# Performance work log

Hardware: AMD Instinct MI355X
Metric: run time of the kernel (lower is better)

Reference implementation:

```python
import jax, jax.numpy as jnp
import numpy as np

HEADS = 16
SEQ_LEN = 2048
EMB = 1024
BATCH = 2


def setup_inputs() -> dict:
    key = jax.random.key(0)
    ks = jax.random.split(key, 5)
    s = 1.0 / np.sqrt(EMB)
    return {
        "x": jax.random.normal(ks[0], (BATCH, SEQ_LEN, EMB), dtype=jnp.float32),
        "Wk": jax.random.normal(ks[1], (EMB, EMB), dtype=jnp.float32) * s,
        "Wq": jax.random.normal(ks[2], (EMB, EMB), dtype=jnp.float32) * s,
        "Wv": jax.random.normal(ks[3], (EMB, EMB), dtype=jnp.float32) * s,
        "Wu": jax.random.normal(ks[4], (EMB, EMB), dtype=jnp.float32) * s,
        "bu": jnp.zeros((EMB,), dtype=jnp.float32),
    }


def reference(x, Wk, Wq, Wv, Wu, bu):
    B, S, E = x.shape
    H = HEADS
    D = E // H
    # projections (torch Linear: y = x @ W.T); split heads -> [B, H, S, D]
    def proj(W):
        return (x @ W.T).reshape(B, S, H, D).transpose(0, 2, 1, 3)
    q, k, v = proj(Wq), proj(Wk), proj(Wv)
    scores = jnp.einsum("bhsd,bhtd->bhst", q, k) / jnp.sqrt(jnp.float32(D))
    causal_mask = jnp.triu(jnp.ones((S, S), dtype=bool), k=1)  # True above diag
    scores = jnp.where(causal_mask, -jnp.inf, scores)
    attn = jax.nn.softmax(scores, axis=-1)
    ctx = jnp.einsum("bhst,bhtd->bhsd", attn, v)  # [B,H,S,D]
    out = ctx.transpose(0, 2, 1, 3).reshape(B, S, E)
    return out @ Wu.T + bu
```

## Files before the change

### kernel.cpp

```cpp
#include <hip/hip_runtime.h>
#include <hip/hip_bf16.h>

#define HEADS 16
#define SEQ   2048
#define EMB   1024
#define BATCH 2
#define DHEAD 64
#define MTOK  (BATCH * SEQ)

typedef __bf16 bf16x8 __attribute__((ext_vector_type(8)));
typedef float  floatx4 __attribute__((ext_vector_type(4)));

__device__ __forceinline__ void gl_lds16(const void* g, void* l) {
  __builtin_amdgcn_global_load_lds((__attribute__((address_space(1))) void*)(g),
                                   (__attribute__((address_space(3))) void*)(l), 16, 0, 0);
}

__device__ __forceinline__ unsigned short f2bf(float f) {
  __bf16 h = (__bf16)f;
  return __builtin_bit_cast(unsigned short, h);
}

__global__ __launch_bounds__(256) void cvt_kernel(
    const float* __restrict__ x,  const float* __restrict__ wq,
    const float* __restrict__ wk, const float* __restrict__ wv,
    const float* __restrict__ wu,
    unsigned short* __restrict__ xb,  unsigned short* __restrict__ wqb,
    unsigned short* __restrict__ wkb, unsigned short* __restrict__ wvb,
    unsigned short* __restrict__ wub) {
  const int g = blockIdx.x * 256 + threadIdx.x;
  const int XG = (MTOK * EMB) / 4;
  const int WG = (EMB * EMB) / 4;
  const float* src; unsigned short* dst; int off;
  if (g < XG) { src = x; dst = xb; off = g; }
  else {
    int t = g - XG; int wsel = t / WG; off = t - wsel * WG;
    const float* ss[4] = {wq, wk, wv, wu};
    unsigned short* dd[4] = {wqb, wkb, wvb, wub};
    src = ss[wsel]; dst = dd[wsel];
  }
  float4 v = ((const float4*)src)[off];
  ushort4 o;
  o.x = f2bf(v.x); o.y = f2bf(v.y); o.z = f2bf(v.z); o.w = f2bf(v.w);
  ((ushort4*)dst)[off] = o;
}

__global__ __launch_bounds__(256) void gemm_qkv(
    const unsigned short* __restrict__ xb,
    const unsigned short* __restrict__ wqb, const unsigned short* __restrict__ wkb,
    const unsigned short* __restrict__ wvb,
    unsigned short* __restrict__ Qb, unsigned short* __restrict__ Kb,
    unsigned short* __restrict__ Vt) {
  constexpr int BM = 128, BN = 128, BK = 64;
  __shared__ unsigned short As[BM * BK];
  __shared__ unsigned short Bs[BN * BK];
  const int z = blockIdx.z;
  const unsigned short* W = (z == 0) ? wqb : (z == 1) ? wkb : wvb;
  const int m0 = blockIdx.x * BM, n0 = blockIdx.y * BN;
  const int tid = threadIdx.x, w = tid >> 6, lane = tid & 63;
  const int quad = lane >> 4, l16 = lane & 15;
  const int wm = w >> 1, wn = w & 1;
  const int srow = lane >> 3;
  const int scol = ((lane & 7) ^ srow) * 8;

  floatx4 acc[4][4] = {};

  for (int kt = 0; kt < EMB / BK; ++kt) {
    const int k0 = kt * BK;
#pragma unroll
    for (int i = 0; i < 4; ++i) {
      int r0 = i * 32 + w * 8;
      gl_lds16(xb + (size_t)(m0 + r0 + srow) * EMB + k0 + scol, &As[r0 * BK]);
      gl_lds16(W  + (size_t)(n0 + r0 + srow) * EMB + k0 + scol, &Bs[r0 * BK]);
    }
    __syncthreads();
    bf16x8 af[4][2], bfv[4][2];
#pragma unroll
    for (int mb = 0; mb < 4; ++mb) {
      int ra = wm * 64 + mb * 16 + l16;
#pragma unroll
      for (int ks = 0; ks < 2; ++ks)
        af[mb][ks] = *(const bf16x8*)&As[ra * BK + (((ks * 4 + quad) ^ (ra & 7)) * 8)];
    }
#pragma unroll
    for (int nb = 0; nb < 4; ++nb) {
      int rb = wn * 64 + nb * 16 + l16;
#pragma unroll
      for (int ks = 0; ks < 2; ++ks)
        bfv[nb][ks] = *(const bf16x8*)&Bs[rb * BK + (((ks * 4 + quad) ^ (rb & 7)) * 8)];
    }
#pragma unroll
    for (int ks = 0; ks < 2; ++ks)
#pragma unroll
      for (int mb = 0; mb < 4; ++mb)
#pragma unroll
        for (int nb = 0; nb < 4; ++nb)
          acc[mb][nb] = __builtin_amdgcn_mfma_f32_16x16x32_bf16(af[mb][ks], bfv[nb][ks], acc[mb][nb], 0, 0, 0);
    __syncthreads();
  }

  if (z < 2) {
    unsigned short* C = (z == 0) ? Qb : Kb;
    const float scale = (z == 0) ? 0.180336876f : 1.0f;
#pragma unroll
    for (int mb = 0; mb < 4; ++mb) {
#pragma unroll
      for (int nb = 0; nb < 4; ++nb) {
        int n = n0 + wn * 64 + nb * 16 + l16;
#pragma unroll
        for (int r = 0; r < 4; ++r) {
          int m = m0 + wm * 64 + mb * 16 + quad * 4 + r;
          C[(size_t)m * EMB + n] = f2bf(acc[mb][nb][r] * scale);
        }
      }
    }
  } else {
#pragma unroll
    for (int mb = 0; mb < 4; ++mb) {
      int mbase = m0 + wm * 64 + mb * 16 + quad * 4;
      int b = mbase >> 11, s = mbase & (SEQ - 1);
#pragma unroll
      for (int nb = 0; nb < 4; ++nb) {
        int n = n0 + wn * 64 + nb * 16 + l16;
        ushort4 o;
        o.x = f2bf(acc[mb][nb][0]); o.y = f2bf(acc[mb][nb][1]);
        o.z = f2bf(acc[mb][nb][2]); o.w = f2bf(acc[mb][nb][3]);
        *(ushort4*)&Vt[((size_t)b * (HEADS * DHEAD) + n) * SEQ + s] = o;
      }
    }
  }
}

__global__ __launch_bounds__(256) void attn_kernel(
    const unsigned short* __restrict__ Qb, const unsigned short* __restrict__ Kb,
    const unsigned short* __restrict__ Vt, unsigned short* __restrict__ ctx) {
  constexpr int KT = 128;
  constexpr int PST = KT + 8;
  __shared__ unsigned short Ks[KT * DHEAD];
  __shared__ unsigned short Vs[DHEAD * KT];
  __shared__ __bf16 Ps[4 * 16 * PST];
  const int pair = blockIdx.x, bh = blockIdx.y;
  const int b = bh >> 4, h = bh & 15;
  const int tid = threadIdx.x, w = tid >> 6, lane = tid & 63;
  const int quad = lane >> 4, l16 = lane & 15;

  const unsigned short* Kbh = Kb + (size_t)b * SEQ * EMB + h * DHEAD;
  const unsigned short* Vbh = Vt + (size_t)bh * DHEAD * SEQ;
  __bf16* Pw = &Ps[w * (16 * PST)];

  int kq[4], kd[4], vd[4], vk[4];
#pragma unroll
  for (int i = 0; i < 4; ++i) {
    int c = i * 256 + tid;
    kq[i] = ((c >> 6) & 7) * 16 + (c & 15);
    kd[i] = ((c >> 9) << 5) + (((c >> 4) & 3) << 3);
    vd[i] = (((c >> 6) & 3) << 4) + (c & 15);
    vk[i] = (((c >> 8) & 3) << 5) + (((c >> 4) & 3) << 3);
  }

  for (int pi = 0; pi < 2; ++pi) {
    const int qt = pi ? (31 - pair) : pair;
    const int q0 = qt * 64;
    const int myrow = q0 + w * 16 + quad * 4;

    const size_t qrow = (size_t)(b * SEQ + q0 + w * 16 + l16) * EMB + h * DHEAD;
    bf16x8 qf[2];
    qf[0] = *(const bf16x8*)&Qb[qrow + quad * 8];
    qf[1] = *(const bf16x8*)&Qb[qrow + 32 + quad * 8];

    float lsum[4] = {0.0f, 0.0f, 0.0f, 0.0f};
    floatx4 acc_o[4] = {};

    const int nkt = (qt + 2) >> 1;
    for (int ktile = 0; ktile < nkt; ++ktile) {
      const int kt0 = ktile * KT;
#pragma unroll
      for (int i = 0; i < 4; ++i) {
        gl_lds16(Kbh + (size_t)(kt0 + kq[i]) * EMB + kd[i], &Ks[(i * 256 + w * 64) * 8]);
        gl_lds16(Vbh + (size_t)vd[i] * SEQ + kt0 + vk[i], &Vs[(i * 256 + w * 64) * 8]);
      }
      __syncthreads();

      floatx4 accs[8] = {};
#pragma unroll
      for (int ks = 0; ks < 2; ++ks)
#pragma unroll
        for (int nb = 0; nb < 8; ++nb) {
          bf16x8 kf = *(const bf16x8*)&Ks[((ks * 8 + nb) * 64 + lane) * 8];
          accs[nb] = __builtin_amdgcn_mfma_f32_16x16x32_bf16(qf[ks], kf, accs[nb], 0, 0, 0);
        }

      if (ktile == nkt - 1) {
#pragma unroll
        for (int nb = 0; nb < 8; ++nb) {
          int col = kt0 + nb * 16 + l16;
#pragma unroll
          for (int r = 0; r < 4; ++r)
            if (col > myrow + r) accs[nb][r] = -1e30f;
        }
      }

#pragma unroll
      for (int r = 0; r < 4; ++r) {
#pragma unroll
        for (int nb = 0; nb < 8; ++nb) {
          float pe = exp2f(accs[nb][r]);
          Pw[(quad * 4 + r) * PST + nb * 16 + l16] = (__bf16)pe;
          lsum[r] += pe;
        }
      }

#pragma unroll
      for (int ks = 0; ks < 4; ++ks) {
        bf16x8 pf = *(const bf16x8*)&Pw[l16 * PST + ks * 32 + quad * 8];
#pragma unroll
        for (int nb = 0; nb < 4; ++nb) {
          bf16x8 vf = *(const bf16x8*)&Vs[((ks * 4 + nb) * 64 + lane) * 8];
          acc_o[nb] = __builtin_amdgcn_mfma_f32_16x16x32_bf16(pf, vf, acc_o[nb], 0, 0, 0);
        }
      }
      __syncthreads();
    }

#pragma unroll
    for (int r = 0; r < 4; ++r) {
      float rs = lsum[r];
      rs += __shfl_xor(rs, 1);
      rs += __shfl_xor(rs, 2);
      rs += __shfl_xor(rs, 4);
      rs += __shfl_xor(rs, 8);
      float inv = 1.0f / rs;
      size_t base = (size_t)(b * SEQ + myrow + r) * EMB + h * DHEAD;
#pragma unroll
      for (int nb = 0; nb < 4; ++nb)
        ctx[base + nb * 16 + l16] = f2bf(acc_o[nb][r] * inv);
    }
  }
}

__global__ __launch_bounds__(256) void gemm_out(
    const unsigned short* __restrict__ ctx, const unsigned short* __restrict__ wub,
    const float* __restrict__ bu, float* __restrict__ out) {
  constexpr int BM = 128, BN = 64, BK = 64;
  __shared__ unsigned short As[BM * BK];
  __shared__ unsigned short Bs[BN * BK];
  const int m0 = blockIdx.x * BM, n0 = blockIdx.y * BN;
  const int tid = threadIdx.x, w = tid >> 6, lane = tid & 63;
  const int quad = lane >> 4, l16 = lane & 15;
  const int wm = w >> 1, wn = w & 1;
  const int srow = lane >> 3;
  const int scol = ((lane & 7) ^ srow) * 8;

  floatx4 acc[4][2] = {};

  for (int kt = 0; kt < EMB / BK; ++kt) {
    const int k0 = kt * BK;
#pragma unroll
    for (int i = 0; i < 4; ++i) {
      int r0 = i * 32 + w * 8;
      gl_lds16(ctx + (size_t)(m0 + r0 + srow) * EMB + k0 + scol, &As[r0 * BK]);
    }
#pragma unroll
    for (int i = 0; i < 2; ++i) {
      int r0 = i * 32 + w * 8;
      gl_lds16(wub + (size_t)(n0 + r0 + srow) * EMB + k0 + scol, &Bs[r0 * BK]);
    }
    __syncthreads();
    bf16x8 af[4][2], bfv[2][2];
#pragma unroll
    for (int mb = 0; mb < 4; ++mb) {
      int ra = wm * 64 + mb * 16 + l16;
#pragma unroll
      for (int ks = 0; ks < 2; ++ks)
        af[mb][ks] = *(const bf16x8*)&As[ra * BK + (((ks * 4 + quad) ^ (ra & 7)) * 8)];
    }
#pragma unroll
    for (int nb = 0; nb < 2; ++nb) {
      int rb = wn * 32 + nb * 16 + l16;
#pragma unroll
      for (int ks = 0; ks < 2; ++ks)
        bfv[nb][ks] = *(const bf16x8*)&Bs[rb * BK + (((ks * 4 + quad) ^ (rb & 7)) * 8)];
    }
#pragma unroll
    for (int ks = 0; ks < 2; ++ks)
#pragma unroll
      for (int mb = 0; mb < 4; ++mb)
#pragma unroll
        for (int nb = 0; nb < 2; ++nb)
          acc[mb][nb] = __builtin_amdgcn_mfma_f32_16x16x32_bf16(af[mb][ks], bfv[nb][ks], acc[mb][nb], 0, 0, 0);
    __syncthreads();
  }

#pragma unroll
  for (int mb = 0; mb < 4; ++mb) {
#pragma unroll
    for (int nb = 0; nb < 2; ++nb) {
      int n = n0 + wn * 32 + nb * 16 + l16;
      float bias = bu[n];
#pragma unroll
      for (int r = 0; r < 4; ++r) {
        int m = m0 + wm * 64 + mb * 16 + quad * 4 + r;
        out[(size_t)m * EMB + n] = acc[mb][nb][r] + bias;
      }
    }
  }
}

extern "C" void kernel_launch(void* const* d_in, const int* in_sizes, int n_in,
                              void* d_out, int out_size, void* d_ws, size_t ws_size,
                              hipStream_t stream) {
  const float* x  = (const float*)d_in[0];
  const float* Wk = (const float*)d_in[1];
  const float* Wq = (const float*)d_in[2];
  const float* Wv = (const float*)d_in[3];
  const float* Wu = (const float*)d_in[4];
  const float* bu = (const float*)d_in[5];

  char* ws = (char*)d_ws;
  const size_t MB1 = 1 << 20;
  unsigned short* xb  = (unsigned short*)(ws + 0);
  unsigned short* wqb = (unsigned short*)(ws + 8  * MB1);
  unsigned short* wkb = (unsigned short*)(ws + 10 * MB1);
  unsigned short* wvb = (unsigned short*)(ws + 12 * MB1);
  unsigned short* wub = (unsigned short*)(ws + 14 * MB1);
  unsigned short* Qb  = (unsigned short*)(ws + 16 * MB1);
  unsigned short* Kb  = (unsigned short*)(ws + 24 * MB1);
  unsigned short* Vt  = (unsigned short*)(ws + 32 * MB1);
  unsigned short* ctx = (unsigned short*)(ws + 40 * MB1);

  cvt_kernel<<<8192, 256, 0, stream>>>(x, Wq, Wk, Wv, Wu, xb, wqb, wkb, wvb, wub);
  gemm_qkv<<<dim3(32, 8, 3), 256, 0, stream>>>(xb, wqb, wkb, wvb, Qb, Kb, Vt);
  attn_kernel<<<dim3(16, 32), 256, 0, stream>>>(Qb, Kb, Vt, ctx);
  gemm_out<<<dim3(32, 16), 256, 0, stream>>>(ctx, wub, bu, (float*)d_out);
}
```

Measured before the change: 189.7 us.

## Fuse QKV weight tiles per block and split attention into per-tile blocks

The QKV GEMM now loads one shared x tile and three 64-wide weight tiles (Q, K, V) per block, so x is staged once for all three projections instead of three times. The grid changes from 32x8x3 to 32x16. The attention kernel drops the paired-tile scheme and launches one block per 64-row query tile, in reverse order so the longest tiles start first, with 64-wide K/V tiles and simpler load indexing. This raises attention block count and parallelism, but each block does more iterations with smaller tiles and more barriers.

Result: slower. 219.8 us (+15.9%).

```diff
diff --git a/kernel.cpp b/kernel.cpp
--- a/kernel.cpp
+++ b/kernel.cpp
@@ -51,19 +51,18 @@
     const unsigned short* __restrict__ wvb,
     unsigned short* __restrict__ Qb, unsigned short* __restrict__ Kb,
     unsigned short* __restrict__ Vt) {
-  constexpr int BM = 128, BN = 128, BK = 64;
+  constexpr int BM = 128, BN = 64, BK = 64;
   __shared__ unsigned short As[BM * BK];
-  __shared__ unsigned short Bs[BN * BK];
-  const int z = blockIdx.z;
-  const unsigned short* W = (z == 0) ? wqb : (z == 1) ? wkb : wvb;
+  __shared__ unsigned short Bs[3 * BN * BK];
   const int m0 = blockIdx.x * BM, n0 = blockIdx.y * BN;
   const int tid = threadIdx.x, w = tid >> 6, lane = tid & 63;
   const int quad = lane >> 4, l16 = lane & 15;
   const int wm = w >> 1, wn = w & 1;
   const int srow = lane >> 3;
   const int scol = ((lane & 7) ^ srow) * 8;
-
-  floatx4 acc[4][4] = {};
+  const unsigned short* Ws[3] = {wqb, wkb, wvb};
+
+  floatx4 acc[3][4][2] = {};
 
   for (int kt = 0; kt < EMB / BK; ++kt) {
     const int k0 = kt * BK;
@@ -71,62 +70,70 @@
     for (int i = 0; i < 4; ++i) {
       int r0 = i * 32 + w * 8;
       gl_lds16(xb + (size_t)(m0 + r0 + srow) * EMB + k0 + scol, &As[r0 * BK]);
-      gl_lds16(W  + (size_t)(n0 + r0 + srow) * EMB + k0 + scol, &Bs[r0 * BK]);
-    }
-    __syncthreads();
-    bf16x8 af[4][2], bfv[4][2];
-#pragma unroll
-    for (int mb = 0; mb < 4; ++mb) {
-      int ra = wm * 64 + mb * 16 + l16;
-#pragma unroll
-      for (int ks = 0; ks < 2; ++ks)
-        af[mb][ks] = *(const bf16x8*)&As[ra * BK + (((ks * 4 + quad) ^ (ra & 7)) * 8)];
-    }
-#pragma unroll
-    for (int nb = 0; nb < 4; ++nb) {
-      int rb = wn * 64 + nb * 16 + l16;
-#pragma unroll
-      for (int ks = 0; ks < 2; ++ks)
-        bfv[nb][ks] = *(const bf16x8*)&Bs[rb * BK + (((ks * 4 + quad) ^ (rb & 7)) * 8)];
-    }
-#pragma unroll
-    for (int ks = 0; ks < 2; ++ks)
-#pragma unroll
-      for (int mb = 0; mb < 4; ++mb)
-#pragma unroll
-        for (int nb = 0; nb < 4; ++nb)
-          acc[mb][nb] = __builtin_amdgcn_mfma_f32_16x16x32_bf16(af[mb][ks], bfv[nb][ks], acc[mb][nb], 0, 0, 0);
-    __syncthreads();
-  }
-
-  if (z < 2) {
+    }
+#pragma unroll
+    for (int z = 0; z < 3; ++z)
+#pragma unroll
+      for (int i = 0; i < 2; ++i) {
+        int r0 = i * 32 + w * 8;
+        gl_lds16(Ws[z] + (size_t)(n0 + r0 + srow) * EMB + k0 + scol,
+                 &Bs[z * (BN * BK) + r0 * BK]);
+      }
+    __syncthreads();
+#pragma unroll
+    for (int ks = 0; ks < 2; ++ks) {
+      bf16x8 af[4];
+#pragma unroll
+      for (int mb = 0; mb < 4; ++mb) {
+        int ra = wm * 64 + mb * 16 + l16;
+        af[mb] = *(const bf16x8*)&As[ra * BK + (((ks * 4 + quad) ^ (ra & 7)) * 8)];
+      }
+#pragma unroll
+      for (int z = 0; z < 3; ++z) {
+        bf16x8 bfv[2];
+#pragma unroll
+        for (int nb = 0; nb < 2; ++nb) {
+          int rb = wn * 32 + nb * 16 + l16;
+          bfv[nb] = *(const bf16x8*)&Bs[z * (BN * BK) + rb * BK + (((ks * 4 + quad) ^ (rb & 7)) * 8)];
+        }
+#pragma unroll
+        for (int mb = 0; mb < 4; ++mb)
+#pragma unroll
+          for (int nb = 0; nb < 2; ++nb)
+            acc[z][mb][nb] = __builtin_amdgcn_mfma_f32_16x16x32_bf16(af[mb], bfv[nb], acc[z][mb][nb], 0, 0, 0);
+      }
+    }
+    __syncthreads();
+  }
+
+#pragma unroll
+  for (int z = 0; z < 2; ++z) {
     unsigned short* C = (z == 0) ? Qb : Kb;
     const float scale = (z == 0) ? 0.180336876f : 1.0f;
 #pragma unroll
     for (int mb = 0; mb < 4; ++mb) {
 #pragma unroll
-      for (int nb = 0; nb < 4; ++nb) {
-        int n = n0 + wn * 64 + nb * 16 + l16;
+      for (int nb = 0; nb < 2; ++nb) {
+        int n = n0 + wn * 32 + nb * 16 + l16;
 #pragma unroll
         for (int r = 0; r < 4; ++r) {
           int m = m0 + wm * 64 + mb * 16 + quad * 4 + r;
-          C[(size_t)m * EMB + n] = f2bf(acc[mb][nb][r] * scale);
+          C[(size_t)m * EMB + n] = f2bf(acc[z][mb][nb][r] * scale);
         }
       }
     }
-  } else {
-#pragma unroll
-    for (int mb = 0; mb < 4; ++mb) {
-      int mbase = m0 + wm * 64 + mb * 16 + quad * 4;
-      int b = mbase >> 11, s = mbase & (SEQ - 1);
-#pragma unroll
-      for (int nb = 0; nb < 4; ++nb) {
-        int n = n0 + wn * 64 + nb * 16 + l16;
-        ushort4 o;
-        o.x = f2bf(acc[mb][nb][0]); o.y = f2bf(acc[mb][nb][1]);
-        o.z = f2bf(acc[mb][nb][2]); o.w = f2bf(acc[mb][nb][3]);
-        *(ushort4*)&Vt[((size_t)b * (HEADS * DHEAD) + n) * SEQ + s] = o;
-      }
+  }
+#pragma unroll
+  for (int mb = 0; mb < 4; ++mb) {
+    int mbase = m0 + wm * 64 + mb * 16 + quad * 4;
+    int b = mbase >> 11, s = mbase & (SEQ - 1);
+#pragma unroll
+    for (int nb = 0; nb < 2; ++nb) {
+      int n = n0 + wn * 32 + nb * 16 + l16;
+      ushort4 o;
+      o.x = f2bf(acc[2][mb][nb][0]); o.y = f2bf(acc[2][mb][nb][1]);
+      o.z = f2bf(acc[2][mb][nb][2]); o.w = f2bf(acc[2][mb][nb][3]);
+      *(ushort4*)&Vt[((size_t)b * (HEADS * DHEAD) + n) * SEQ + s] = o;
     }
   }
 }
@@ -134,13 +141,14 @@
 __global__ __launch_bounds__(256) void attn_kernel(
     const unsigned short* __restrict__ Qb, const unsigned short* __restrict__ Kb,
     const unsigned short* __restrict__ Vt, unsigned short* __restrict__ ctx) {
-  constexpr int KT = 128;
-  constexpr int PST = KT + 8;
+  constexpr int KT = 64;
+  constexpr int PST = KT + 12;
   __shared__ unsigned short Ks[KT * DHEAD];
   __shared__ unsigned short Vs[DHEAD * KT];
   __shared__ __bf16 Ps[4 * 16 * PST];
-  const int pair = blockIdx.x, bh = blockIdx.y;
+  const int qt = 31 - blockIdx.x, bh = blockIdx.y;
   const int b = bh >> 4, h = bh & 15;
+  const int q0 = qt * 64;
   const int tid = threadIdx.x, w = tid >> 6, lane = tid & 63;
   const int quad = lane >> 4, l16 = lane & 15;
 
@@ -148,93 +156,80 @@
   const unsigned short* Vbh = Vt + (size_t)bh * DHEAD * SEQ;
   __bf16* Pw = &Ps[w * (16 * PST)];
 
-  int kq[4], kd[4], vd[4], vk[4];
-#pragma unroll
-  for (int i = 0; i < 4; ++i) {
-    int c = i * 256 + tid;
-    kq[i] = ((c >> 6) & 7) * 16 + (c & 15);
-    kd[i] = ((c >> 9) << 5) + (((c >> 4) & 3) << 3);
-    vd[i] = (((c >> 6) & 3) << 4) + (c & 15);
-    vk[i] = (((c >> 8) & 3) << 5) + (((c >> 4) & 3) << 3);
-  }
-
-  for (int pi = 0; pi < 2; ++pi) {
-    const int qt = pi ? (31 - pair) : pair;
-    const int q0 = qt * 64;
-    const int myrow = q0 + w * 16 + quad * 4;
-
-    const size_t qrow = (size_t)(b * SEQ + q0 + w * 16 + l16) * EMB + h * DHEAD;
-    bf16x8 qf[2];
-    qf[0] = *(const bf16x8*)&Qb[qrow + quad * 8];
-    qf[1] = *(const bf16x8*)&Qb[qrow + 32 + quad * 8];
-
-    float lsum[4] = {0.0f, 0.0f, 0.0f, 0.0f};
-    floatx4 acc_o[4] = {};
-
-    const int nkt = (qt + 2) >> 1;
-    for (int ktile = 0; ktile < nkt; ++ktile) {
-      const int kt0 = ktile * KT;
-#pragma unroll
-      for (int i = 0; i < 4; ++i) {
-        gl_lds16(Kbh + (size_t)(kt0 + kq[i]) * EMB + kd[i], &Ks[(i * 256 + w * 64) * 8]);
-        gl_lds16(Vbh + (size_t)vd[i] * SEQ + kt0 + vk[i], &Vs[(i * 256 + w * 64) * 8]);
-      }
-      __syncthreads();
-
-      floatx4 accs[8] = {};
-#pragma unroll
-      for (int ks = 0; ks < 2; ++ks)
-#pragma unroll
-        for (int nb = 0; nb < 8; ++nb) {
-          bf16x8 kf = *(const bf16x8*)&Ks[((ks * 8 + nb) * 64 + lane) * 8];
-          accs[nb] = __builtin_amdgcn_mfma_f32_16x16x32_bf16(qf[ks], kf, accs[nb], 0, 0, 0);
-        }
-
-      if (ktile == nkt - 1) {
-#pragma unroll
-        for (int nb = 0; nb < 8; ++nb) {
-          int col = kt0 + nb * 16 + l16;
-#pragma unroll
-          for (int r = 0; r < 4; ++r)
-            if (col > myrow + r) accs[nb][r] = -1e30f;
-        }
-      }
-
-#pragma unroll
-      for (int r = 0; r < 4; ++r) {
-#pragma unroll
-        for (int nb = 0; nb < 8; ++nb) {
-          float pe = exp2f(accs[nb][r]);
-          Pw[(quad * 4 + r) * PST + nb * 16 + l16] = (__bf16)pe;
-          lsum[r] += pe;
-        }
-      }
-
-#pragma unroll
-      for (int ks = 0; ks < 4; ++ks) {
-        bf16x8 pf = *(const bf16x8*)&Pw[l16 * PST + ks * 32 + quad * 8];
-#pragma unroll
-        for (int nb = 0; nb < 4; ++nb) {
-          bf16x8 vf = *(const bf16x8*)&Vs[((ks * 4 + nb) * 64 + lane) * 8];
-          acc_o[nb] = __builtin_amdgcn_mfma_f32_16x16x32_bf16(pf, vf, acc_o[nb], 0, 0, 0);
-        }
-      }
-      __syncthreads();
+  const int krow = w * 16 + l16;
+  const int dc0 = quad * 8, dc1 = 32 + quad * 8;
+
+  const int myrow = q0 + w * 16 + quad * 4;
+  const size_t qrow = (size_t)(b * SEQ + q0 + w * 16 + l16) * EMB + h * DHEAD;
+  bf16x8 qf[2];
+  qf[0] = *(const bf16x8*)&Qb[qrow + quad * 8];
+  qf[1] = *(const bf16x8*)&Qb[qrow + 32 + quad * 8];
+
+  float lsum[4] = {0.0f, 0.0f, 0.0f, 0.0f};
+  floatx4 acc_o[4] = {};
+
+  const int nkt = qt + 1;
+  for (int ktile = 0; ktile < nkt; ++ktile) {
+    const int kt0 = ktile * KT;
+    gl_lds16(Kbh + (size_t)(kt0 + krow) * EMB + dc0, &Ks[(w * 64 + lane) * 8]);
+    gl_lds16(Kbh + (size_t)(kt0 + krow) * EMB + dc1, &Ks[((4 + w) * 64 + lane) * 8]);
+    gl_lds16(Vbh + (size_t)krow * SEQ + kt0 + dc0, &Vs[(w * 64 + lane) * 8]);
+    gl_lds16(Vbh + (size_t)krow * SEQ + kt0 + dc1, &Vs[((4 + w) * 64 + lane) * 8]);
+    __syncthreads();
+
+    floatx4 accs[4] = {};
+#pragma unroll
+    for (int ks = 0; ks < 2; ++ks)
+#pragma unroll
+      for (int nb = 0; nb < 4; ++nb) {
+        bf16x8 kf = *(const bf16x8*)&Ks[((ks * 4 + nb) * 64 + lane) * 8];
+        accs[nb] = __builtin_amdgcn_mfma_f32_16x16x32_bf16(qf[ks], kf, accs[nb], 0, 0, 0);
+      }
+
+    if (ktile == nkt - 1) {
+#pragma unroll
+      for (int nb = 0; nb < 4; ++nb) {
+        int col = kt0 + nb * 16 + l16;
+#pragma unroll
+        for (int r = 0; r < 4; ++r)
+          if (col > myrow + r) accs[nb][r] = -1e30f;
+      }
     }
 
 #pragma unroll
     for (int r = 0; r < 4; ++r) {
-      float rs = lsum[r];
-      rs += __shfl_xor(rs, 1);
-      rs += __shfl_xor(rs, 2);
-      rs += __shfl_xor(rs, 4);
-      rs += __shfl_xor(rs, 8);
-      float inv = 1.0f / rs;
-      size_t base = (size_t)(b * SEQ + myrow + r) * EMB + h * DHEAD;
-#pragma unroll
-      for (int nb = 0; nb < 4; ++nb)
-        ctx[base + nb * 16 + l16] = f2bf(acc_o[nb][r] * inv);
-    }
+#pragma unroll
+      for (int nb = 0; nb < 4; ++nb) {
+        float pe = exp2f(accs[nb][r]);
+        Pw[(quad * 4 + r) * PST + nb * 16 + l16] = (__bf16)pe;
+        lsum[r] += pe;
+      }
+    }
+
+#pragma unroll
+    for (int ks = 0; ks < 2; ++ks) {
+      bf16x8 pf = *(const bf16x8*)&Pw[l16 * PST + ks * 32 + quad * 8];
+#pragma unroll
+      for (int nb = 0; nb < 4; ++nb) {
+        bf16x8 vf = *(const bf16x8*)&Vs[((ks * 4 + nb) * 64 + lane) * 8];
+        acc_o[nb] = __builtin_amdgcn_mfma_f32_16x16x32_bf16(pf, vf, acc_o[nb], 0, 0, 0);
+      }
+    }
+    __syncthreads();
+  }
+
+#pragma unroll
+  for (int r = 0; r < 4; ++r) {
+    float rs = lsum[r];
+    rs += __shfl_xor(rs, 1);
+    rs += __shfl_xor(rs, 2);
+    rs += __shfl_xor(rs, 4);
+    rs += __shfl_xor(rs, 8);
+    float inv = 1.0f / rs;
+    size_t base = (size_t)(b * SEQ + myrow + r) * EMB + h * DHEAD;
+#pragma unroll
+    for (int nb = 0; nb < 4; ++nb)
+      ctx[base + nb * 16 + l16] = f2bf(acc_o[nb][r] * inv);
   }
 }
 
@@ -329,7 +324,7 @@
   unsigned short* ctx = (unsigned short*)(ws + 40 * MB1);
 
   cvt_kernel<<<8192, 256, 0, stream>>>(x, Wq, Wk, Wv, Wu, xb, wqb, wkb, wvb, wub);
-  gemm_qkv<<<dim3(32, 8, 3), 256, 0, stream>>>(xb, wqb, wkb, wvb, Qb, Kb, Vt);
-  attn_kernel<<<dim3(16, 32), 256, 0, stream>>>(Qb, Kb, Vt, ctx);
+  gemm_qkv<<<dim3(32, 16), 256, 0, stream>>>(xb, wqb, wkb, wvb, Qb, Kb, Vt);
+  attn_kernel<<<dim3(32, 32), 256, 0, stream>>>(Qb, Kb, Vt, ctx);
   gemm_out<<<dim3(32, 16), 256, 0, stream>>>(ctx, wub, bu, (float*)d_out);
 }
```
